# Kernel tuning notes

Hardware: AMD Instinct MI355X
Metric: run time of the kernel (lower is better)

Reference implementation:

```python
import jax, jax.numpy as jnp
import numpy as np

HEADS = 8
DIM_HEAD = 160
QUERY_DIM = 1280
INNER = HEADS * DIM_HEAD  # 1280
B, S = 2, 4096


def setup_inputs() -> dict:
    key = jax.random.key(0)
    ks = jax.random.split(key, 7)
    scale = 0.02
    return {
        "hidden_states": jax.random.normal(ks[0], (B, QUERY_DIM, 1, S), jnp.float32),
        "context": jax.random.normal(ks[1], (B, QUERY_DIM, 1, S), jnp.float32),
        "mask": jnp.zeros((B, S, 1, 1), jnp.float32),
        "Wq": jax.random.normal(ks[2], (INNER, QUERY_DIM), jnp.float32) * scale,
        "Wk": jax.random.normal(ks[3], (INNER, QUERY_DIM), jnp.float32) * scale,
        "Wv": jax.random.normal(ks[4], (INNER, QUERY_DIM), jnp.float32) * scale,
        "Wout": jax.random.normal(ks[5], (QUERY_DIM, INNER), jnp.float32) * scale,
        "bout": jnp.zeros((QUERY_DIM,), jnp.float32),
    }


def reference(hidden_states, context, mask, Wq, Wk, Wv, Wout, bout):
    # hidden_states/context: [B, C, 1, S]; 1x1 conv == channel-dim matmul.
    x = hidden_states[:, :, 0, :]  # [B, C, Sq]
    c = context[:, :, 0, :]        # [B, C, Sk]
    scale = DIM_HEAD ** (-0.5)

    q = jnp.einsum("oc,bcs->bos", Wq, x)  # [B, inner, Sq]
    k = jnp.einsum("oc,bcs->bos", Wk, c)  # [B, inner, Sk]
    v = jnp.einsum("oc,bcs->bos", Wv, c)  # [B, inner, Sk]

    bsz, _, sq = q.shape
    sk = k.shape[-1]
    qh = q.reshape(bsz, HEADS, DIM_HEAD, sq)
    kh = k.reshape(bsz, HEADS, DIM_HEAD, sk)
    vh = v.reshape(bsz, HEADS, DIM_HEAD, sk)

    # split_einsum: per-head q^T k * scale, mask added per kv position,
    # softmax over kv dim. Vectorized over heads here (same math).
    scores = jnp.einsum("bhdq,bhdk->bhqk", qh, kh) * scale  # [B,H,Sq,Sk]
    scores = scores + mask[:, 0:, 0, 0][:, None, None, :]   # mask over kv
    weights = jax.nn.softmax(scores, axis=-1)
    attn = jnp.einsum("bhqk,bhdk->bhdq", weights, vh)       # [B,H,Dh,Sq]
    attn = attn.reshape(bsz, INNER, sq)

    out = jnp.einsum("oc,bcs->bos", Wout, attn) + bout[None, :, None]
    return out[:, :, None, :]  # [B, C, 1, Sq]
```

## Files before the change

kernel.cpp:

```cpp
#include <hip/hip_runtime.h>
#include <hip/hip_bf16.h>
#include <math.h>

#define B_   2
#define S_   4096
#define H_   8
#define D_   160
#define QD_  1280
#define SCALE 0.07905694150420949f
#define LOG2E 1.4426950408889634f

typedef unsigned short ushort_t;
typedef __attribute__((ext_vector_type(8))) short short8;
typedef __attribute__((ext_vector_type(4))) float f32x4;

#define MFMA16(a, b, c) __builtin_amdgcn_mfma_f32_16x16x32_bf16(a, b, c, 0, 0, 0)

__device__ __forceinline__ ushort_t f2bf(float f) {
  unsigned u = __float_as_uint(f);
  u += 0x7fffu + ((u >> 16) & 1u);
  return (ushort_t)(u >> 16);
}
__device__ __forceinline__ ushort_t f2bf_fast(float f) {
  return (ushort_t)((__float_as_uint(f) + 0x8000u) >> 16);
}

__device__ __forceinline__ void gload_lds16(const ushort_t* g, ushort_t* l) {
  __builtin_amdgcn_global_load_lds(
      (const __attribute__((address_space(1))) unsigned int*)(g),
      (__attribute__((address_space(3))) unsigned int*)(l), 16, 0, 0);
}

template <int CTRL>
__device__ __forceinline__ float dpp_mov(float x) {
  return __int_as_float(
      __builtin_amdgcn_update_dpp(0, __float_as_int(x), CTRL, 0xF, 0xF, true));
}
__device__ __forceinline__ float row_sum16(float x) {
  x += dpp_mov<0xB1>(x);
  x += dpp_mov<0x4E>(x);
  x += dpp_mov<0x124>(x);
  x += dpp_mov<0x128>(x);
  return x;
}

__global__ __launch_bounds__(256) void transpose_cvt(
    const float* __restrict__ src, ushort_t* __restrict__ dst)
{
  const int b = blockIdx.z;
  const int s0 = blockIdx.x * 32;
  const int c0 = blockIdx.y * 32;
  __shared__ float T[32][33];
  const int t = threadIdx.x;
  const int sl = t & 31, cr = t >> 5;
#pragma unroll
  for (int i = 0; i < 4; ++i)
    T[cr + i * 8][sl] = src[((size_t)b * QD_ + c0 + cr + i * 8) * S_ + s0 + sl];
  __syncthreads();
  const int cl = (t & 7) * 4, sr = t >> 3;
  ushort4 v;
  v.x = f2bf(T[cl + 0][sr]);
  v.y = f2bf(T[cl + 1][sr]);
  v.z = f2bf(T[cl + 2][sr]);
  v.w = f2bf(T[cl + 3][sr]);
  *(ushort4*)(dst + ((size_t)b * S_ + s0 + sr) * QD_ + c0 + cl) = v;
}

__global__ __launch_bounds__(256) void cvt_w(
    const float* __restrict__ w0, const float* __restrict__ w1,
    const float* __restrict__ w2, const float* __restrict__ w3,
    ushort_t* __restrict__ o0, ushort_t* __restrict__ o1,
    ushort_t* __restrict__ o2, ushort_t* __restrict__ o3)
{
  const int which = blockIdx.y;
  const float* s = which == 0 ? w0 : which == 1 ? w1 : which == 2 ? w2 : w3;
  ushort_t* d    = which == 0 ? o0 : which == 1 ? o1 : which == 2 ? o2 : o3;
  const size_t i = ((size_t)blockIdx.x * 256 + threadIdx.x) * 4;
  const float4 f = *(const float4*)(s + i);
  ushort4 v;
  v.x = f2bf(f.x); v.y = f2bf(f.y); v.z = f2bf(f.z); v.w = f2bf(f.w);
  *(ushort4*)(d + i) = v;
}

#define GBM 128
#define GBN 128
#define GBK 32

__global__ __launch_bounds__(256) void gemm_mfma(
    const ushort_t* __restrict__ A, const ushort_t* __restrict__ B,
    void* __restrict__ Cp, const float* __restrict__ bias,
    int M, int N, int K, int mode,
    size_t strideA, size_t strideB, size_t strideC,
    int cm, int cn)
{
  const int bz = blockIdx.z;
  const int nx = gridDim.x;
  const int tiles_x = nx / cn;
  const int orig = blockIdx.x + nx * blockIdx.y;
  const int xcd = orig & 7;
  const int idx = orig >> 3;
  const int trow = xcd / tiles_x, tcol = xcd - trow * tiles_x;
  const int bm = trow * cm + idx / cn;
  const int bn = tcol * cn + idx % cn;
  const int m0 = bm * GBM;
  const int n0 = bn * GBN;

  const ushort_t* __restrict__ Ab = A + (size_t)bz * strideA;
  const ushort_t* __restrict__ Bb = B + (size_t)bz * strideB;

  __shared__ ushort_t As[GBM * GBK];
  __shared__ ushort_t Bs[GBN * GBK];

  const int t = threadIdx.x;
  const int wid = t >> 6, lane = t & 63;
  const int l16 = lane & 15, quad = lane >> 4;
  const int wm = (wid >> 1) * 64, wn = (wid & 1) * 64;

  f32x4 acc[4][4];
#pragma unroll
  for (int i = 0; i < 4; ++i)
#pragma unroll
    for (int j = 0; j < 4; ++j) acc[i][j] = {0.f, 0.f, 0.f, 0.f};

  for (int k0 = 0; k0 < K; k0 += GBK) {
    __syncthreads();
#pragma unroll
    for (int i = 0; i < 2; ++i) {
      const int G = (i * 4 + wid) * 64 + lane;
      const int r = G >> 2, sl = G & 3;
      const int g = sl ^ (r & 3);
      gload_lds16(Ab + (size_t)(m0 + r) * K + k0 + g * 8, &As[(i * 4 + wid) * 512]);
      gload_lds16(Bb + (size_t)(n0 + r) * K + k0 + g * 8, &Bs[(i * 4 + wid) * 512]);
    }
    __syncthreads();

    short8 af[4], bfr[4];
#pragma unroll
    for (int mt = 0; mt < 4; ++mt) {
      const int r = wm + mt * 16 + l16;
      af[mt] = *(const short8*)&As[r * 32 + ((quad ^ (r & 3)) << 3)];
    }
#pragma unroll
    for (int nt = 0; nt < 4; ++nt) {
      const int r = wn + nt * 16 + l16;
      bfr[nt] = *(const short8*)&Bs[r * 32 + ((quad ^ (r & 3)) << 3)];
    }
#pragma unroll
    for (int mt = 0; mt < 4; ++mt)
#pragma unroll
      for (int nt = 0; nt < 4; ++nt)
        acc[mt][nt] = MFMA16(af[mt], bfr[nt], acc[mt][nt]);
  }

  if (mode == 0) {
    ushort_t* C = (ushort_t*)Cp + (size_t)bz * strideC;
#pragma unroll
    for (int mt = 0; mt < 4; ++mt)
#pragma unroll
      for (int r = 0; r < 4; ++r) {
        const int row = m0 + wm + mt * 16 + quad * 4 + r;
        ushort_t* cr = C + (size_t)row * N + n0 + wn + l16;
#pragma unroll
        for (int nt = 0; nt < 4; ++nt) cr[nt * 16] = f2bf_fast(acc[mt][nt][r]);
      }
  } else {
    float* C = (float*)Cp + (size_t)bz * strideC;
#pragma unroll
    for (int mt = 0; mt < 4; ++mt)
#pragma unroll
      for (int r = 0; r < 4; ++r) {
        const int row = m0 + wm + mt * 16 + quad * 4 + r;
        const float bv = bias[row];
        float* cr = C + (size_t)row * N + n0 + wn + l16;
#pragma unroll
        for (int nt = 0; nt < 4; ++nt) cr[nt * 16] = acc[mt][nt][r] + bv;
      }
  }
}

#define TQ 128
#define TK 64
#define KTSTR 168
#define VTSTR 72
#define PSTR  72

__global__ __launch_bounds__(256, 2) void flash_attn_mfma(
    const ushort_t* __restrict__ qws, const ushort_t* __restrict__ kws,
    const ushort_t* __restrict__ vws, const float* __restrict__ mask,
    ushort_t* __restrict__ attn_out)
{
  const int b  = blockIdx.z;
  const int orig = blockIdx.x + 32 * blockIdx.y;
  const int swz  = ((orig & 7) << 5) | (orig >> 3);
  const int q0 = (swz & 31) * TQ;
  const int h  = swz >> 5;
  const int t  = threadIdx.x;
  const int wid  = t >> 6;
  const int lane = t & 63;
  const int l16  = lane & 15;
  const int quad = lane >> 4;

  __shared__ __align__(16) ushort_t smem[31744];
  ushort_t* Kt = smem;
  ushort_t* Vt = smem + 1344 * 8;
  ushort_t* Pp = smem + 2816 * 8;

  int goff[11];
#pragma unroll
  for (int jj = 0; jj < 11; ++jj) {
    const int j = jj * 4 + wid;
    const int slot = j * 64 + lane;
    int off;
    if (j < 21) {
      const int r = slot / 21, c = slot - r * 21;
      off = (c < 20) ? r * QD_ + c * 8 : 0;
    } else {
      const int vs = slot - 1344;
      const int r = vs / 9, c = vs - r * 9;
      off = (c < 8 && r < 160) ? r * S_ + c * 8 : 0;
    }
    goff[jj] = off;
  }

  const ushort_t* kg = kws + (size_t)b * S_ * QD_ + h * D_;
  const ushort_t* vg = vws + ((size_t)b * QD_ + h * D_) * S_;

  short8 aq[2][5];
#pragma unroll
  for (int mt = 0; mt < 2; ++mt) {
    const ushort_t* qrow =
        qws + ((size_t)(b * S_ + q0 + wid * 32 + mt * 16 + l16)) * QD_ + h * D_;
#pragma unroll
    for (int dc = 0; dc < 5; ++dc)
      aq[mt][dc] = *(const short8*)(qrow + dc * 32 + quad * 8);
  }

#pragma unroll
  for (int jj = 0; jj < 6; ++jj) {
    const int j = jj * 4 + wid;
    if (j < 21) gload_lds16(kg + goff[jj], &smem[(size_t)j * 512]);
  }
#pragma unroll
  for (int jj = 5; jj < 11; ++jj) {
    const int j = jj * 4 + wid;
    if (j >= 21) gload_lds16(vg + goff[jj], &smem[(size_t)j * 512]);
  }

  f32x4 Oa[2][10];
#pragma unroll
  for (int mt = 0; mt < 2; ++mt)
#pragma unroll
    for (int nt = 0; nt < 10; ++nt) Oa[mt][nt] = {0.f, 0.f, 0.f, 0.f};
  float lpart[2][4] = {{0.f, 0.f, 0.f, 0.f}, {0.f, 0.f, 0.f, 0.f}};
  const float SC2 = SCALE * LOG2E;

  const int pswz = quad << 4;
  const int prsw = (l16 >> 2) << 4;

  for (int kp0 = 0; kp0 < S_; kp0 += TK) {
    asm volatile("s_waitcnt vmcnt(5)" ::: "memory");
    __builtin_amdgcn_sched_barrier(0);
    __builtin_amdgcn_s_barrier();
    __builtin_amdgcn_sched_barrier(0);

    float mv[4];
#pragma unroll
    for (int c = 0; c < 4; ++c)
      mv[c] = mask[b * S_ + kp0 + c * 16 + l16] * LOG2E;

    f32x4 s[2][4];
#pragma unroll
    for (int mt = 0; mt < 2; ++mt)
#pragma unroll
      for (int c = 0; c < 4; ++c) s[mt][c] = {0.f, 0.f, 0.f, 0.f};
    __builtin_amdgcn_s_setprio(1);
#pragma unroll
    for (int dc = 0; dc < 5; ++dc) {
      short8 bb[4];
#pragma unroll
      for (int c = 0; c < 4; ++c)
        bb[c] = *(const short8*)&Kt[(c * 16 + l16) * KTSTR + dc * 32 + quad * 8];
#pragma unroll
      for (int mt = 0; mt < 2; ++mt)
#pragma unroll
        for (int c = 0; c < 4; ++c)
          s[mt][c] = MFMA16(aq[mt][dc], bb[c], s[mt][c]);
    }
    __builtin_amdgcn_s_setprio(0);

    ushort_t* pw = Pp + wid * (32 * PSTR);
#pragma unroll
    for (int mt = 0; mt < 2; ++mt)
#pragma unroll
      for (int r = 0; r < 4; ++r) {
        const float p0 = exp2f(s[mt][0][r] * SC2 + mv[0]);
        const float p1 = exp2f(s[mt][1][r] * SC2 + mv[1]);
        const float p2 = exp2f(s[mt][2][r] * SC2 + mv[2]);
        const float p3 = exp2f(s[mt][3][r] * SC2 + mv[3]);
        lpart[mt][r] += (p0 + p1) + (p2 + p3);
        ushort_t* prow = pw + (mt * 16 + quad * 4 + r) * PSTR;
        prow[(pswz ^  0) + l16] = f2bf_fast(p0);
        prow[(pswz ^ 16) + l16] = f2bf_fast(p1);
        prow[(pswz ^ 32) + l16] = f2bf_fast(p2);
        prow[(pswz ^ 48) + l16] = f2bf_fast(p3);
      }

    short8 ap[2][2];
#pragma unroll
    for (int mt = 0; mt < 2; ++mt) {
#pragma unroll
      for (int ks = 0; ks < 2; ++ks)
        ap[mt][ks] = *(const short8*)
            &Pp[wid * (32 * PSTR) + (mt * 16 + l16) * PSTR +
                ((ks * 32 + quad * 8) ^ prsw)];
    }

    __syncthreads();

    const int kn = kp0 + TK;
    if (kn < S_) {
      const ushort_t* kgn = kg + (size_t)kn * QD_;
#pragma unroll
      for (int jj = 0; jj < 6; ++jj) {
        const int j = jj * 4 + wid;
        if (j < 21) gload_lds16(kgn + goff[jj], &smem[(size_t)j * 512]);
      }
      __builtin_amdgcn_sched_barrier(0);
    }

    __builtin_amdgcn_s_setprio(1);
#pragma unroll
    for (int nt = 0; nt < 10; ++nt) {
      const short8 bv0 = *(const short8*)&Vt[(nt * 16 + l16) * VTSTR + quad * 8];
      const short8 bv1 = *(const short8*)&Vt[(nt * 16 + l16) * VTSTR + 32 + quad * 8];
#pragma unroll
      for (int mt = 0; mt < 2; ++mt) {
        Oa[mt][nt] = MFMA16(ap[mt][0], bv0, Oa[mt][nt]);
        Oa[mt][nt] = MFMA16(ap[mt][1], bv1, Oa[mt][nt]);
      }
    }
    __builtin_amdgcn_s_setprio(0);

    __builtin_amdgcn_sched_barrier(0);
    __builtin_amdgcn_s_barrier();
    __builtin_amdgcn_sched_barrier(0);

    if (kn < S_) {
      const ushort_t* vgn = vg + kn;
#pragma unroll
      for (int jj = 5; jj < 11; ++jj) {
        const int j = jj * 4 + wid;
        if (j >= 21) gload_lds16(vgn + goff[jj], &smem[(size_t)j * 512]);
      }
    }
  }

#pragma unroll
  for (int mt = 0; mt < 2; ++mt)
#pragma unroll
    for (int r = 0; r < 4; ++r) {
      const float l = row_sum16(lpart[mt][r]);
      const float inv = 1.f / l;
      const int qq = q0 + wid * 32 + mt * 16 + quad * 4 + r;
      ushort_t* orow = attn_out + ((size_t)(b * S_ + qq)) * QD_ + h * D_;
#pragma unroll
      for (int nt = 0; nt < 10; ++nt)
        orow[nt * 16 + l16] = f2bf_fast(Oa[mt][nt][r] * inv);
    }
}

extern "C" void kernel_launch(void* const* d_in, const int* in_sizes, int n_in,
                              void* d_out, int out_size, void* d_ws, size_t ws_size,
                              hipStream_t stream) {
  const float* x    = (const float*)d_in[0];
  const float* c    = (const float*)d_in[1];
  const float* mask = (const float*)d_in[2];
  const float* Wq   = (const float*)d_in[3];
  const float* Wk   = (const float*)d_in[4];
  const float* Wv   = (const float*)d_in[5];
  const float* Wout = (const float*)d_in[6];
  const float* bout = (const float*)d_in[7];
  float* out = (float*)d_out;

  const size_t PB   = (size_t)S_ * QD_;
  const size_t NELT = (size_t)B_ * PB;
  const size_t WN   = (size_t)QD_ * QD_;

  ushort_t* Xt    = (ushort_t*)d_ws;
  ushort_t* Ct    = Xt + NELT;
  ushort_t* Wqb   = Ct + NELT;
  ushort_t* Wkb   = Wqb + WN;
  ushort_t* Wvb   = Wkb + WN;
  ushort_t* Woutb = Wvb + WN;
  ushort_t* q_ws  = Woutb + WN;
  ushort_t* k_ws  = q_ws + NELT;
  ushort_t* v_ws  = k_ws + NELT;
  ushort_t* attn_ws = v_ws + NELT;

  const dim3 tgrid(S_ / 32, QD_ / 32, B_);
  transpose_cvt<<<tgrid, 256, 0, stream>>>(x, Xt);
  transpose_cvt<<<tgrid, 256, 0, stream>>>(c, Ct);
  cvt_w<<<dim3(WN / 1024, 4, 1), 256, 0, stream>>>(Wq, Wk, Wv, Wout,
                                                   Wqb, Wkb, Wvb, Woutb);

  const dim3 gq(QD_ / GBN, S_ / GBM, B_);
  gemm_mfma<<<gq, 256, 0, stream>>>(Xt, Wqb, q_ws, nullptr,
                                    S_, QD_, QD_, 0, PB, 0, PB, 4, 10);
  gemm_mfma<<<gq, 256, 0, stream>>>(Ct, Wkb, k_ws, nullptr,
                                    S_, QD_, QD_, 0, PB, 0, PB, 4, 10);
  const dim3 gv(S_ / GBN, QD_ / GBM, B_);
  gemm_mfma<<<gv, 256, 0, stream>>>(Wvb, Ct, v_ws, nullptr,
                                    QD_, S_, QD_, 0, 0, PB, PB, 5, 8);

  const dim3 agrid(S_ / TQ, H_, B_);
  flash_attn_mfma<<<agrid, 256, 0, stream>>>(q_ws, k_ws, v_ws, mask, attn_ws);

  gemm_mfma<<<gv, 256, 0, stream>>>(Woutb, attn_ws, out, bout,
                                    QD_, S_, QD_, 1, 0, PB, PB, 5, 8);
}
```

Before: 617.3 us.

## Double-buffer GEMM LDS loads and merge QKV projections and transposes into single launches

Both GEMM kernels now use two LDS buffers and issue the global-to-LDS loads for the next K tile before computing the current one. This replaces the two-barrier load/compute loop and is meant to hide global load latency. The Q, K and V projections now run in one gemm_qkv launch, and the two input transposes in one launch, which cuts launch overhead and lets the work of the separate launches run concurrently. The cost is doubled LDS use per block, which may lower occupancy.

```diff
diff --git a/kernel.cpp b/kernel.cpp
--- a/kernel.cpp
+++ b/kernel.cpp
@@ -44,10 +44,14 @@
   return x;
 }
 
-__global__ __launch_bounds__(256) void transpose_cvt(
-    const float* __restrict__ src, ushort_t* __restrict__ dst)
+__global__ __launch_bounds__(256) void transpose_cvt2(
+    const float* __restrict__ xs, const float* __restrict__ cs,
+    ushort_t* __restrict__ Xt, ushort_t* __restrict__ Ct)
 {
-  const int b = blockIdx.z;
+  const int z = blockIdx.z;
+  const int b = z & 1;
+  const float* src = (z < 2) ? xs : cs;
+  ushort_t* dst    = (z < 2) ? Xt : Ct;
   const int s0 = blockIdx.x * 32;
   const int c0 = blockIdx.y * 32;
   __shared__ float T[32][33];
@@ -86,6 +90,106 @@
 #define GBN 128
 #define GBK 32
 
+#define GEMM_STAGE(tt, p, Abp, Bbp, Kv)                                        \
+  {                                                                            \
+    const int k0s = (tt) * GBK;                                                \
+    _Pragma("unroll")                                                          \
+    for (int i = 0; i < 2; ++i) {                                              \
+      const int G = (i * 4 + wid) * 64 + lane;                                 \
+      const int r = G >> 2, sl = G & 3;                                        \
+      const int g = sl ^ (r & 3);                                              \
+      gload_lds16(Abp + (size_t)(m0 + r) * (Kv) + k0s + g * 8,                 \
+                  &As[p][(i * 4 + wid) * 512]);                                \
+      gload_lds16(Bbp + (size_t)(n0 + r) * (Kv) + k0s + g * 8,                 \
+                  &Bs[p][(i * 4 + wid) * 512]);                                \
+    }                                                                          \
+  }
+
+__global__ __launch_bounds__(256) void gemm_qkv(
+    const ushort_t* __restrict__ Xt, const ushort_t* __restrict__ Ct,
+    const ushort_t* __restrict__ Wqb, const ushort_t* __restrict__ Wkb,
+    const ushort_t* __restrict__ Wvb,
+    ushort_t* __restrict__ q_ws, ushort_t* __restrict__ k_ws,
+    ushort_t* __restrict__ v_ws)
+{
+  const size_t PB = (size_t)S_ * QD_;
+  const int which = blockIdx.z >> 1, b = blockIdx.z & 1;
+  const ushort_t* Ab;
+  const ushort_t* Bb;
+  ushort_t* Cb;
+  int Nv, nx, cm, cn;
+  if (which == 0) {
+    Ab = Xt + (size_t)b * PB; Bb = Wqb; Cb = q_ws + (size_t)b * PB;
+    Nv = QD_; nx = 10; cm = 4; cn = 10;
+  } else if (which == 1) {
+    Ab = Ct + (size_t)b * PB; Bb = Wkb; Cb = k_ws + (size_t)b * PB;
+    Nv = QD_; nx = 10; cm = 4; cn = 10;
+  } else {
+    Ab = Wvb; Bb = Ct + (size_t)b * PB; Cb = v_ws + (size_t)b * PB;
+    Nv = S_; nx = 32; cm = 5; cn = 8;
+  }
+  const int tiles_x = nx / cn;
+  const int orig = blockIdx.x;
+  const int xcd = orig & 7, idx = orig >> 3;
+  const int trow = xcd / tiles_x, tcol = xcd - trow * tiles_x;
+  const int m0 = (trow * cm + idx / cn) * GBM;
+  const int n0 = (tcol * cn + idx % cn) * GBN;
+
+  __shared__ ushort_t As[2][GBM * GBK];
+  __shared__ ushort_t Bs[2][GBN * GBK];
+
+  const int t = threadIdx.x;
+  const int wid = t >> 6, lane = t & 63;
+  const int l16 = lane & 15, quad = lane >> 4;
+  const int wm = (wid >> 1) * 64, wn = (wid & 1) * 64;
+
+  f32x4 acc[4][4];
+#pragma unroll
+  for (int i = 0; i < 4; ++i)
+#pragma unroll
+    for (int j = 0; j < 4; ++j) acc[i][j] = {0.f, 0.f, 0.f, 0.f};
+
+  const int NIT = QD_ / GBK;
+  GEMM_STAGE(0, 0, Ab, Bb, QD_);
+  for (int it = 0; it < NIT; ++it) {
+    asm volatile("s_waitcnt vmcnt(0)" ::: "memory");
+    __builtin_amdgcn_sched_barrier(0);
+    __builtin_amdgcn_s_barrier();
+    __builtin_amdgcn_sched_barrier(0);
+    if (it + 1 < NIT) {
+      GEMM_STAGE(it + 1, (it + 1) & 1, Ab, Bb, QD_);
+      __builtin_amdgcn_sched_barrier(0);
+    }
+    const int p = it & 1;
+    short8 af[4], bfr[4];
+#pragma unroll
+    for (int mt = 0; mt < 4; ++mt) {
+      const int r = wm + mt * 16 + l16;
+      af[mt] = *(const short8*)&As[p][r * 32 + ((quad ^ (r & 3)) << 3)];
+    }
+#pragma unroll
+    for (int nt = 0; nt < 4; ++nt) {
+      const int r = wn + nt * 16 + l16;
+      bfr[nt] = *(const short8*)&Bs[p][r * 32 + ((quad ^ (r & 3)) << 3)];
+    }
+#pragma unroll
+    for (int mt = 0; mt < 4; ++mt)
+#pragma unroll
+      for (int nt = 0; nt < 4; ++nt)
+        acc[mt][nt] = MFMA16(af[mt], bfr[nt], acc[mt][nt]);
+  }
+
+#pragma unroll
+  for (int mt = 0; mt < 4; ++mt)
+#pragma unroll
+    for (int r = 0; r < 4; ++r) {
+      const int row = m0 + wm + mt * 16 + quad * 4 + r;
+      ushort_t* cr = Cb + (size_t)row * Nv + n0 + wn + l16;
+#pragma unroll
+      for (int nt = 0; nt < 4; ++nt) cr[nt * 16] = f2bf_fast(acc[mt][nt][r]);
+    }
+}
+
 __global__ __launch_bounds__(256) void gemm_mfma(
     const ushort_t* __restrict__ A, const ushort_t* __restrict__ B,
     void* __restrict__ Cp, const float* __restrict__ bias,
@@ -100,16 +204,14 @@
   const int xcd = orig & 7;
   const int idx = orig >> 3;
   const int trow = xcd / tiles_x, tcol = xcd - trow * tiles_x;
-  const int bm = trow * cm + idx / cn;
-  const int bn = tcol * cn + idx % cn;
-  const int m0 = bm * GBM;
-  const int n0 = bn * GBN;
+  const int m0 = (trow * cm + idx / cn) * GBM;
+  const int n0 = (tcol * cn + idx % cn) * GBN;
 
   const ushort_t* __restrict__ Ab = A + (size_t)bz * strideA;
   const ushort_t* __restrict__ Bb = B + (size_t)bz * strideB;
 
-  __shared__ ushort_t As[GBM * GBK];
-  __shared__ ushort_t Bs[GBN * GBK];
+  __shared__ ushort_t As[2][GBM * GBK];
+  __shared__ ushort_t Bs[2][GBN * GBK];
 
   const int t = threadIdx.x;
   const int wid = t >> 6, lane = t & 63;
@@ -122,28 +224,28 @@
 #pragma unroll
     for (int j = 0; j < 4; ++j) acc[i][j] = {0.f, 0.f, 0.f, 0.f};
 
-  for (int k0 = 0; k0 < K; k0 += GBK) {
-    __syncthreads();
-#pragma unroll
-    for (int i = 0; i < 2; ++i) {
-      const int G = (i * 4 + wid) * 64 + lane;
-      const int r = G >> 2, sl = G & 3;
-      const int g = sl ^ (r & 3);
-      gload_lds16(Ab + (size_t)(m0 + r) * K + k0 + g * 8, &As[(i * 4 + wid) * 512]);
-      gload_lds16(Bb + (size_t)(n0 + r) * K + k0 + g * 8, &Bs[(i * 4 + wid) * 512]);
-    }
-    __syncthreads();
-
+  const int NIT = K / GBK;
+  GEMM_STAGE(0, 0, Ab, Bb, K);
+  for (int it = 0; it < NIT; ++it) {
+    asm volatile("s_waitcnt vmcnt(0)" ::: "memory");
+    __builtin_amdgcn_sched_barrier(0);
+    __builtin_amdgcn_s_barrier();
+    __builtin_amdgcn_sched_barrier(0);
+    if (it + 1 < NIT) {
+      GEMM_STAGE(it + 1, (it + 1) & 1, Ab, Bb, K);
+      __builtin_amdgcn_sched_barrier(0);
+    }
+    const int p = it & 1;
     short8 af[4], bfr[4];
 #pragma unroll
     for (int mt = 0; mt < 4; ++mt) {
       const int r = wm + mt * 16 + l16;
-      af[mt] = *(const short8*)&As[r * 32 + ((quad ^ (r & 3)) << 3)];
+      af[mt] = *(const short8*)&As[p][r * 32 + ((quad ^ (r & 3)) << 3)];
     }
 #pragma unroll
     for (int nt = 0; nt < 4; ++nt) {
       const int r = wn + nt * 16 + l16;
-      bfr[nt] = *(const short8*)&Bs[r * 32 + ((quad ^ (r & 3)) << 3)];
+      bfr[nt] = *(const short8*)&Bs[p][r * 32 + ((quad ^ (r & 3)) << 3)];
     }
 #pragma unroll
     for (int mt = 0; mt < 4; ++mt)
@@ -397,24 +499,18 @@
   ushort_t* v_ws  = k_ws + NELT;
   ushort_t* attn_ws = v_ws + NELT;
 
-  const dim3 tgrid(S_ / 32, QD_ / 32, B_);
-  transpose_cvt<<<tgrid, 256, 0, stream>>>(x, Xt);
-  transpose_cvt<<<tgrid, 256, 0, stream>>>(c, Ct);
+  const dim3 tgrid(S_ / 32, QD_ / 32, 2 * B_);
+  transpose_cvt2<<<tgrid, 256, 0, stream>>>(x, c, Xt, Ct);
   cvt_w<<<dim3(WN / 1024, 4, 1), 256, 0, stream>>>(Wq, Wk, Wv, Wout,
                                                    Wqb, Wkb, Wvb, Woutb);
 
-  const dim3 gq(QD_ / GBN, S_ / GBM, B_);
-  gemm_mfma<<<gq, 256, 0, stream>>>(Xt, Wqb, q_ws, nullptr,
-                                    S_, QD_, QD_, 0, PB, 0, PB, 4, 10);
-  gemm_mfma<<<gq, 256, 0, stream>>>(Ct, Wkb, k_ws, nullptr,
-                                    S_, QD_, QD_, 0, PB, 0, PB, 4, 10);
-  const dim3 gv(S_ / GBN, QD_ / GBM, B_);
-  gemm_mfma<<<gv, 256, 0, stream>>>(Wvb, Ct, v_ws, nullptr,
-                                    QD_, S_, QD_, 0, 0, PB, PB, 5, 8);
+  gemm_qkv<<<dim3(320, 1, 6), 256, 0, stream>>>(Xt, Ct, Wqb, Wkb, Wvb,
+                                                q_ws, k_ws, v_ws);
 
   const dim3 agrid(S_ / TQ, H_, B_);
   flash_attn_mfma<<<agrid, 256, 0, stream>>>(q_ws, k_ws, v_ws, mask, attn_ws);
 
+  const dim3 gv(S_ / GBN, QD_ / GBM, B_);
   gemm_mfma<<<gv, 256, 0, stream>>>(Woutb, attn_ws, out, bout,
                                     QD_, S_, QD_, 1, 0, PB, PB, 5, 8);
 }
```

After: 540.9 us. 12.4% less time.
